# Optimization experiments

Hardware: AMD Instinct MI355X
Metric: run time of the kernel (lower is better)

Reference implementation:

```python
import jax, jax.numpy as jnp
import numpy as np

H = 256
W = 256
RADIUS = 1.5
TAU = 1.0
EPS = 1e-8


def _ndc_grid(h, w):
    ys, xs = jnp.meshgrid(jnp.arange(h, dtype=jnp.float32), jnp.arange(w, dtype=jnp.float32), indexing='ij')
    xs = xs / (w - 1) * 2.0 - 1.0
    ys = ys / (h - 1) * 2.0 - 1.0
    return jnp.stack([xs.ravel(), ys.ravel()], 0)  # [2, N]


def _make_rt(key, b, v):
    # near-identity extrinsics: identity rotation + small random translation
    t = jax.random.normal(key, (b, v, 3), dtype=jnp.float32) * 0.05
    rt = jnp.tile(jnp.eye(4, dtype=jnp.float32), (b, v, 1, 1))
    rt = rt.at[:, :, :3, 3].set(t)
    return rt


def setup_inputs() -> dict:
    key = jax.random.key(0)
    ks = jax.random.split(key, 4)
    B, V, C = 2, 3, 32
    depths = jax.random.uniform(ks[0], (B, V, 1, H, W), jnp.float32, 1.0, 3.0)
    feats = jax.random.normal(ks[1], (B, V, C, H, W), jnp.float32)
    K = jnp.tile(jnp.eye(4, dtype=jnp.float32), (B, 1, 1))
    K = K.at[:, 0, 0].set(1.2).at[:, 1, 1].set(1.2)  # NDC-space focal lengths
    src_RTs = _make_rt(ks[2], B, V)
    src_RTinvs = jnp.linalg.inv(src_RTs)
    dst_RTs = _make_rt(ks[3], B, 1)
    dst_RTinvs = jnp.linalg.inv(dst_RTs)
    return {"depths": depths, "feats": feats, "K": K, "src_RTs": src_RTs,
            "src_RTinvs": src_RTinvs, "dst_RTs": dst_RTs, "dst_RTinvs": dst_RTinvs}


def _view_to_world(depth, K_inv, RTinv):
    # depth: [BV, 1, N] -> world homogeneous coords [BV, 4, N]
    grid = _ndc_grid(H, W)                                      # [2, N]
    xy = grid[None] * depth                                     # [BV, 2, N]
    pc = jnp.concatenate([xy, depth, jnp.ones_like(depth)], 1)  # [BV, 4, N]
    cam = jnp.einsum('bij,bjn->bin', K_inv, pc)
    return jnp.einsum('bij,bjn->bin', RTinv, cam)


def _world_to_view(wrld, K, RT):
    cam = jnp.einsum('bij,bjn->bin', RT, wrld)
    proj = jnp.einsum('bij,bjn->bin', K, cam)
    z = proj[:, 2:3]
    xy = proj[:, 0:2] / (z + EPS)
    xy = jnp.where(z <= 0.0, -10.0, xy)       # invalid points pushed off-screen
    return jnp.concatenate([xy, z], 1)        # [BV, 3, N]


def _splatter(pc, feats, radius):
    # pc: [BV, N, 3] (x_ndc, y_ndc, depth); feats: [BV, C, N]
    BV, N, _ = pc.shape
    C = feats.shape[1]
    x, y, z = pc[..., 0], pc[..., 1], pc[..., 2]
    px = (x + 1.0) * 0.5 * (W - 1)
    py = (y + 1.0) * 0.5 * (H - 1)
    offs = jnp.array([[dy, dx] for dy in (-1, 0, 1) for dx in (-1, 0, 1)], dtype=jnp.float32)
    ix = jnp.round(px)[..., None] + offs[:, 1]     # [BV, N, 9]
    iy = jnp.round(py)[..., None] + offs[:, 0]
    dist = jnp.sqrt((ix - px[..., None]) ** 2 + (iy - py[..., None]) ** 2 + EPS)
    w_r = jnp.maximum(0.0, 1.0 - dist / radius)    # radius-based falloff
    valid = (ix >= 0) & (ix < W) & (iy >= 0) & (iy < H) & (z[..., None] > 0)
    w_d = jnp.exp(-TAU * z)[..., None]             # depth-aware (soft z-buffer) weight
    w = w_r * w_d * valid.astype(w_r.dtype)        # [BV, N, 9]
    idx = iy.astype(jnp.int32).clip(0, H - 1) * W + ix.astype(jnp.int32).clip(0, W - 1)
    flat = (jnp.arange(BV, dtype=jnp.int32)[:, None, None] * (H * W) + idx).reshape(-1)
    w_sum = jax.ops.segment_sum(w.reshape(-1), flat, num_segments=BV * H * W)
    fw = (feats[:, :, :, None] * w[:, None, :, :]).transpose(0, 2, 3, 1).reshape(-1, C)
    f_sum = jax.ops.segment_sum(fw, flat, num_segments=BV * H * W)
    z_sum = jax.ops.segment_sum((z[..., None] * w).reshape(-1), flat, num_segments=BV * H * W)
    out_f = (f_sum / (w_sum[:, None] + EPS)).reshape(BV, H, W, C).transpose(0, 3, 1, 2)
    out_d = (z_sum / (w_sum + EPS)).reshape(BV, 1, H, W)
    return out_f, out_d


def reference(depths, feats, K, src_RTs, src_RTinvs, dst_RTs, dst_RTinvs):
    B, V, C = feats.shape[0], feats.shape[1], feats.shape[2]
    N = H * W
    d = depths.reshape(B * V, 1, N)
    f = feats.reshape(B * V, C, N)
    K_bv = jnp.repeat(K, V, axis=0)
    K_inv_bv = jnp.repeat(jnp.linalg.inv(K), V, axis=0)
    src_rtinv = src_RTinvs.reshape(B * V, 4, 4)
    dst_rt = jnp.repeat(dst_RTs[:, 0], V, axis=0)
    wrld = _view_to_world(d, K_inv_bv, src_rtinv)      # view -> world per source view
    sampler = _world_to_view(wrld, K_bv, dst_rt)       # world -> target view [BV,3,N]
    pc = sampler.transpose(0, 2, 1)                    # [BV, N, 3]
    prj_f, prj_d = _splatter(pc, f, RADIUS)
    return prj_f.reshape(B, V, C, H, W), prj_d.reshape(B, V, 1, H, W)
```

## Files before the change

kernel.cpp:

```cpp
#include <hip/hip_runtime.h>
#include <hip/hip_fp16.h>
#include <math.h>

#define H 256
#define W 256
#define HW (H * W)
#define B 2
#define V 3
#define BV (B * V)
#define C 32
#define RADIUS 1.5f
#define TAU 1.0f
#define EPS 1e-8f

#define NPIX (BV * HW)
#define NBLK (NPIX / 256)

#define GW 258
#define GH 258
#define NCELL (BV * GH * GW)
#define NSUMS ((NCELL + 255) / 256)
#define ROWCAP 64

__device__ __forceinline__ int swizzle_block(int bid) {
    return (bid & 7) * (NBLK / 8) + (bid >> 3);
}

__global__ void setup_kernel(const float* __restrict__ Kmat,
                             const float* __restrict__ srcRTinv,
                             const float* __restrict__ dstRT,
                             float* __restrict__ Mbuf) {
    int bv = threadIdx.x;
    if (bv >= BV) return;
    int b = bv / V;

    float a[4][8];
    for (int i = 0; i < 4; i++)
        for (int j = 0; j < 4; j++) {
            a[i][j] = Kmat[b * 16 + i * 4 + j];
            a[i][4 + j] = (i == j) ? 1.0f : 0.0f;
        }
    for (int col = 0; col < 4; col++) {
        int piv = col;
        float best = fabsf(a[col][col]);
        for (int r = col + 1; r < 4; r++) {
            float v = fabsf(a[r][col]);
            if (v > best) { best = v; piv = r; }
        }
        if (piv != col) {
            for (int j = 0; j < 8; j++) {
                float t = a[col][j]; a[col][j] = a[piv][j]; a[piv][j] = t;
            }
        }
        float s = 1.0f / a[col][col];
        for (int j = 0; j < 8; j++) a[col][j] *= s;
        for (int r = 0; r < 4; r++) {
            if (r == col) continue;
            float m = a[r][col];
            for (int j = 0; j < 8; j++) a[r][j] -= m * a[col][j];
        }
    }
    float Kinv[16];
    for (int i = 0; i < 4; i++)
        for (int j = 0; j < 4; j++) Kinv[i * 4 + j] = a[i][4 + j];

    float T1[16];
    const float* S = srcRTinv + bv * 16;
    for (int i = 0; i < 4; i++)
        for (int j = 0; j < 4; j++) {
            float acc = 0.0f;
            for (int k = 0; k < 4; k++) acc += S[i * 4 + k] * Kinv[k * 4 + j];
            T1[i * 4 + j] = acc;
        }
    float T2[16];
    const float* D = dstRT + b * 16;
    for (int i = 0; i < 4; i++)
        for (int j = 0; j < 4; j++) {
            float acc = 0.0f;
            for (int k = 0; k < 4; k++) acc += D[i * 4 + k] * T1[k * 4 + j];
            T2[i * 4 + j] = acc;
        }
    const float* Kb = Kmat + b * 16;
    for (int i = 0; i < 4; i++)
        for (int j = 0; j < 4; j++) {
            float acc = 0.0f;
            for (int k = 0; k < 4; k++) acc += Kb[i * 4 + k] * T2[k * 4 + j];
            Mbuf[bv * 16 + i * 4 + j] = acc;
        }
}

__global__ __launch_bounds__(256) void project_count_kernel(
    const float* __restrict__ depths, const float* __restrict__ Mbuf,
    float4* __restrict__ staging, int2* __restrict__ meta) {
    int gid = swizzle_block(blockIdx.x) * 256 + threadIdx.x;
    int bv = gid >> 16;
    int n = gid & (HW - 1);

    float xn = (float)(n & (W - 1)) * (2.0f / (W - 1)) - 1.0f;
    float yn = (float)(n >> 8)      * (2.0f / (H - 1)) - 1.0f;
    float d = depths[gid];
    const float* M = Mbuf + bv * 16;
    float X = xn * d, Y = yn * d;
    float p0 = M[0] * X + M[1] * Y + M[2] * d + M[3];
    float p1 = M[4] * X + M[5] * Y + M[6] * d + M[7];
    float z  = M[8] * X + M[9] * Y + M[10] * d + M[11];

    int cell = -1;
    float px = 0.0f, py = 0.0f;
    if (z > 0.0f) {
        float inv = 1.0f / (z + EPS);
        px = (p0 * inv + 1.0f) * 0.5f * (float)(W - 1);
        py = (p1 * inv + 1.0f) * 0.5f * (float)(H - 1);
        float rx = rintf(px), ry = rintf(py);
        if (rx >= -1.0f && rx <= (float)W && ry >= -1.0f && ry <= (float)H) {
            cell = bv * (GH * GW) + ((int)ry + 1) * GW + ((int)rx + 1);
            atomicAdd(&meta[cell].y, 1);
        }
    }
    staging[gid] = make_float4(px, py, z, __int_as_float(cell));
}

__global__ __launch_bounds__(256) void alloc1_kernel(int2* __restrict__ meta,
                                                     int* __restrict__ bsum) {
    int i = blockIdx.x * 256 + threadIdx.x;
    int c = (i < NCELL) ? meta[i].y : 0;
    int lane = threadIdx.x & 63;
    int wid = threadIdx.x >> 6;
    int x = c;
#pragma unroll
    for (int dlt = 1; dlt < 64; dlt <<= 1) {
        int y = __shfl_up(x, dlt);
        if (lane >= dlt) x += y;
    }
    __shared__ int wsum[4];
    __shared__ int wbase[4];
    if (lane == 63) wsum[wid] = x;
    __syncthreads();
    if (threadIdx.x == 0) {
        int s0 = wsum[0], s1 = wsum[1], s2 = wsum[2], s3 = wsum[3];
        wbase[0] = 0; wbase[1] = s0; wbase[2] = s0 + s1; wbase[3] = s0 + s1 + s2;
        bsum[blockIdx.x] = s0 + s1 + s2 + s3;
    }
    __syncthreads();
    if (i <= NCELL) meta[i].x = wbase[wid] + (x - c);
}

__global__ __launch_bounds__(256) void alloc2_kernel(int* __restrict__ bsum) {
    __shared__ int wsum[4];
    __shared__ int wbase[4];
    __shared__ int carry_s;
    int tid = threadIdx.x;
    int lane = tid & 63;
    int wid = tid >> 6;
    if (tid == 0) carry_s = 0;
    __syncthreads();
    const int nchunk = (NSUMS + 255) / 256;
    for (int ch = 0; ch < nchunk; ch++) {
        int i = ch * 256 + tid;
        int c = (i < NSUMS) ? bsum[i] : 0;
        int x = c;
#pragma unroll
        for (int dlt = 1; dlt < 64; dlt <<= 1) {
            int y = __shfl_up(x, dlt);
            if (lane >= dlt) x += y;
        }
        if (lane == 63) wsum[wid] = x;
        __syncthreads();
        if (tid == 0) {
            int cr = carry_s;
            int s0 = wsum[0], s1 = wsum[1], s2 = wsum[2], s3 = wsum[3];
            wbase[0] = cr; wbase[1] = cr + s0; wbase[2] = cr + s0 + s1;
            wbase[3] = cr + s0 + s1 + s2;
            carry_s = cr + s0 + s1 + s2 + s3;
        }
        __syncthreads();
        if (i < NSUMS) bsum[i] = wbase[wid] + (x - c);
        __syncthreads();
    }
}

__global__ __launch_bounds__(256) void fill_kernel(
    const float* __restrict__ feats, const float4* __restrict__ staging,
    const int* __restrict__ bsum, int2* __restrict__ meta,
    float4* __restrict__ entries16, uint4* __restrict__ entriesF) {
    __shared__ float sm[C][257];
    int blk = blockIdx.x;
    int bv = blk >> 8;
    int n0 = (blk & 255) << 8;
    int tid = threadIdx.x;
    const float* src = feats + (size_t)bv * C * HW + n0;
#pragma unroll
    for (int c = 0; c < C; c++) sm[c][tid] = src[(size_t)c * HW + tid];
    __syncthreads();

    int gid = (bv << 16) | (n0 + tid);
    float4 s = staging[gid];
    int cell = __float_as_int(s.w);
    if (cell < 0) return;
    int pos = bsum[cell >> 8] + atomicAdd(&meta[cell].x, 1);

    float wd = expf(-TAU * s.z);
    entries16[pos] = make_float4(s.x, s.y, s.z, wd);

    uint4* dst = entriesF + (size_t)pos * 4;
#pragma unroll
    for (int g = 0; g < 4; g++) {
        __half2 h0 = __floats2half2_rn(sm[g * 8 + 0][tid], sm[g * 8 + 1][tid]);
        __half2 h1 = __floats2half2_rn(sm[g * 8 + 2][tid], sm[g * 8 + 3][tid]);
        __half2 h2 = __floats2half2_rn(sm[g * 8 + 4][tid], sm[g * 8 + 5][tid]);
        __half2 h3 = __floats2half2_rn(sm[g * 8 + 6][tid], sm[g * 8 + 7][tid]);
        uint4 pk;
        pk.x = *(unsigned int*)&h0;
        pk.y = *(unsigned int*)&h1;
        pk.z = *(unsigned int*)&h2;
        pk.w = *(unsigned int*)&h3;
        dst[g] = pk;
    }
}

__global__ __launch_bounds__(256) void gather_kernel(
    const float4* __restrict__ entries16, const uint4* __restrict__ entriesF,
    const int2* __restrict__ meta, const int* __restrict__ bsum,
    float* __restrict__ out) {
    __shared__ float4 lds_e[18][ROWCAP];
    __shared__ int cs_s[18][19];
    __shared__ int row_rs[18];
    __shared__ int row_stg[18];

    int sblk = swizzle_block(blockIdx.x);
    int bv = sblk >> 8;
    int t = sblk & 255;
    int ty0 = (t >> 4) << 4;
    int tx0 = (t & 15) << 4;
    int tid = threadIdx.x;
    int cellbase = bv * (GH * GW);

    for (int i = tid; i < 18 * 19; i += 256) {
        int hr = i / 19, lc = i - hr * 19;
        int cg = cellbase + (ty0 + hr) * GW + (tx0 + lc);
        int2 m = meta[cg];
        cs_s[hr][lc] = bsum[cg >> 8] + m.x - m.y;
    }
    __syncthreads();
    if (tid < 18) {
        int rs = cs_s[tid][0];
        row_rs[tid] = rs;
        row_stg[tid] = min(cs_s[tid][18] - rs, ROWCAP);
    }
    __syncthreads();
    {
        int wid = tid >> 6, lane = tid & 63;
        for (int hr = wid; hr < 18; hr += 4)
            if (lane < row_stg[hr])
                lds_e[hr][lane] = entries16[row_rs[hr] + lane];
    }
    __syncthreads();

    int lx = tid & 15, ly = tid >> 4;
    float qx = (float)(tx0 + lx);
    float qy = (float)(ty0 + ly);

    float wsum = 0.0f, zwsum = 0.0f;
    float facc[C];
#pragma unroll
    for (int c = 0; c < C; c++) facc[c] = 0.0f;

    auto accum = [&](float4 v, int pos) {
        float ddx = qx - v.x, ddy = qy - v.y;
        float d2 = ddx * ddx + ddy * ddy + EPS;
        if (d2 < RADIUS * RADIUS) {
            float dist = sqrtf(d2);
            float wr = 1.0f - dist * (1.0f / RADIUS);
            float w = wr * v.w;
            wsum += w;
            zwsum += v.z * w;
            const uint4* fp = entriesF + (size_t)pos * 4;
#pragma unroll
            for (int g = 0; g < 4; g++) {
                uint4 fv = fp[g];
                const __half2* h2 = (const __half2*)&fv;
#pragma unroll
                for (int k = 0; k < 4; k++) {
                    float2 f2 = __half22float2(h2[k]);
                    facc[g * 8 + 2 * k]     = fmaf(w, f2.x, facc[g * 8 + 2 * k]);
                    facc[g * 8 + 2 * k + 1] = fmaf(w, f2.y, facc[g * 8 + 2 * k + 1]);
                }
            }
        }
    };

#pragma unroll
    for (int dy = 0; dy < 3; dy++) {
        int hr = ly + dy;
        int s = cs_s[hr][lx];
        int e = cs_s[hr][lx + 3];
        int rs = row_rs[hr];
        int se = rs + row_stg[hr];
        int e1 = min(e, se);
        for (int pos = s; pos < e1; ++pos)
            accum(lds_e[hr][pos - rs], pos);
        for (int pos = max(s, se); pos < e; ++pos)
            accum(entries16[pos], pos);
    }

    int q = ((ty0 + ly) << 8) | (tx0 + lx);
    int gid = (bv << 16) | q;
    float invw = 1.0f / (wsum + EPS);
    float* ob = out + (size_t)bv * C * HW + q;
#pragma unroll
    for (int c = 0; c < C; c++) ob[(size_t)c * HW] = facc[c] * invw;
    out[(size_t)BV * C * HW + gid] = zwsum * invw;
}

extern "C" void kernel_launch(void* const* d_in, const int* in_sizes, int n_in,
                              void* d_out, int out_size, void* d_ws, size_t ws_size,
                              hipStream_t stream) {
    const float* depths   = (const float*)d_in[0];
    const float* feats    = (const float*)d_in[1];
    const float* Kmat     = (const float*)d_in[2];
    const float* srcRTinv = (const float*)d_in[4];
    const float* dstRT    = (const float*)d_in[5];
    float* out = (float*)d_out;

    char* ws = (char*)d_ws;
    size_t off_entriesF = 0;
    size_t off_entries16 = off_entriesF + (size_t)NPIX * 64;
    size_t off_staging = off_entries16 + (size_t)NPIX * 16;
    size_t off_meta = off_staging + (size_t)NPIX * 16;
    size_t off_bsum = off_meta + (size_t)(NCELL + 1) * 8;
    size_t off_M = off_bsum + (size_t)NSUMS * 4 + 16;
    size_t needed = off_M + (size_t)BV * 16 * 4;

    if (ws_size < needed) {
        hipMemsetAsync(d_out, 0, (size_t)out_size * 4, stream);
        return;
    }

    uint4* entriesF   = (uint4*)(ws + off_entriesF);
    float4* entries16 = (float4*)(ws + off_entries16);
    float4* staging   = (float4*)(ws + off_staging);
    int2* meta        = (int2*)(ws + off_meta);
    int* bsum         = (int*)(ws + off_bsum);
    float* Mbuf       = (float*)(ws + off_M);

    hipMemsetAsync(meta, 0, (size_t)(NCELL + 1) * 8, stream);
    setup_kernel<<<1, 64, 0, stream>>>(Kmat, srcRTinv, dstRT, Mbuf);
    project_count_kernel<<<NBLK, 256, 0, stream>>>(depths, Mbuf, staging, meta);
    alloc1_kernel<<<NSUMS, 256, 0, stream>>>(meta, bsum);
    alloc2_kernel<<<1, 256, 0, stream>>>(bsum);
    fill_kernel<<<NBLK, 256, 0, stream>>>(feats, staging, bsum, meta,
                                          entries16, entriesF);
    gather_kernel<<<NBLK, 256, 0, stream>>>(entries16, entriesF, meta, bsum,
                                            out);
}
```

Before: 183.9 us.

## Stage half-precision splat features into LDS alongside positions in gather kernel

The gather kernel now stages each tile's entry features (fp16, 64 bytes per entry, padded to a stride of 5 uint4) in shared memory next to the positions. Entries are packed into one flat buffer of up to 384 entries with per-row offsets, instead of a fixed 64 entries per row. This is meant to replace repeated scattered global feature reads by neighbouring threads with LDS reads. In exchange it uses about 36KB of LDS per block, which may lower occupancy, and it adds a serial prefix computation on one thread.

New measurement: 183.6 us. No clear change (-0.2%).

```diff
diff --git a/kernel.cpp b/kernel.cpp
--- a/kernel.cpp
+++ b/kernel.cpp
@@ -20,7 +20,7 @@
 #define GH 258
 #define NCELL (BV * GH * GW)
 #define NSUMS ((NCELL + 255) / 256)
-#define ROWCAP 64
+#define ECAP 384
 
 __device__ __forceinline__ int swizzle_block(int bid) {
     return (bid & 7) * (NBLK / 8) + (bid >> 3);
@@ -222,10 +222,12 @@
     const float4* __restrict__ entries16, const uint4* __restrict__ entriesF,
     const int2* __restrict__ meta, const int* __restrict__ bsum,
     float* __restrict__ out) {
-    __shared__ float4 lds_e[18][ROWCAP];
     __shared__ int cs_s[18][19];
     __shared__ int row_rs[18];
-    __shared__ int row_stg[18];
+    __shared__ int row_off[18];
+    __shared__ int row_sl[18];
+    __shared__ float4 lds_e[ECAP];
+    __shared__ uint4 lds_f[ECAP * 5];
 
     int sblk = swizzle_block(blockIdx.x);
     int bv = sblk >> 8;
@@ -242,17 +244,30 @@
         cs_s[hr][lc] = bsum[cg >> 8] + m.x - m.y;
     }
     __syncthreads();
-    if (tid < 18) {
-        int rs = cs_s[tid][0];
-        row_rs[tid] = rs;
-        row_stg[tid] = min(cs_s[tid][18] - rs, ROWCAP);
+    if (tid == 0) {
+        int off = 0;
+        for (int hr = 0; hr < 18; hr++) {
+            int rs = cs_s[hr][0];
+            int len = cs_s[hr][18] - rs;
+            int sl = min(len, ECAP - off);
+            if (sl < 0) sl = 0;
+            row_rs[hr] = rs;
+            row_off[hr] = off;
+            row_sl[hr] = sl;
+            off += sl;
+        }
     }
     __syncthreads();
     {
         int wid = tid >> 6, lane = tid & 63;
-        for (int hr = wid; hr < 18; hr += 4)
-            if (lane < row_stg[hr])
-                lds_e[hr][lane] = entries16[row_rs[hr] + lane];
+        for (int hr = wid; hr < 18; hr += 4) {
+            int rs = row_rs[hr], off = row_off[hr], sl = row_sl[hr];
+            for (int j = lane; j < sl; j += 64)
+                lds_e[off + j] = entries16[rs + j];
+            int j0 = lane >> 2, g = lane & 3;
+            for (int j = j0; j < sl; j += 16)
+                lds_f[(off + j) * 5 + g] = entriesF[(size_t)(rs + j) * 4 + g];
+        }
     }
     __syncthreads();
 
@@ -265,7 +280,29 @@
 #pragma unroll
     for (int c = 0; c < C; c++) facc[c] = 0.0f;
 
-    auto accum = [&](float4 v, int pos) {
+    auto accum_lds = [&](float4 v, int li) {
+        float ddx = qx - v.x, ddy = qy - v.y;
+        float d2 = ddx * ddx + ddy * ddy + EPS;
+        if (d2 < RADIUS * RADIUS) {
+            float dist = sqrtf(d2);
+            float wr = 1.0f - dist * (1.0f / RADIUS);
+            float w = wr * v.w;
+            wsum += w;
+            zwsum += v.z * w;
+#pragma unroll
+            for (int g = 0; g < 4; g++) {
+                uint4 fv = lds_f[li * 5 + g];
+                const __half2* h2 = (const __half2*)&fv;
+#pragma unroll
+                for (int k = 0; k < 4; k++) {
+                    float2 f2 = __half22float2(h2[k]);
+                    facc[g * 8 + 2 * k]     = fmaf(w, f2.x, facc[g * 8 + 2 * k]);
+                    facc[g * 8 + 2 * k + 1] = fmaf(w, f2.y, facc[g * 8 + 2 * k + 1]);
+                }
+            }
+        }
+    };
+    auto accum_glb = [&](float4 v, int pos) {
         float ddx = qx - v.x, ddy = qy - v.y;
         float d2 = ddx * ddx + ddy * ddy + EPS;
         if (d2 < RADIUS * RADIUS) {
@@ -295,12 +332,15 @@
         int s = cs_s[hr][lx];
         int e = cs_s[hr][lx + 3];
         int rs = row_rs[hr];
-        int se = rs + row_stg[hr];
-        int e1 = min(e, se);
-        for (int pos = s; pos < e1; ++pos)
-            accum(lds_e[hr][pos - rs], pos);
-        for (int pos = max(s, se); pos < e; ++pos)
-            accum(entries16[pos], pos);
+        int off = row_off[hr];
+        int sEnd = rs + row_sl[hr];
+        int e1 = min(e, sEnd);
+        for (int pos = s; pos < e1; ++pos) {
+            int li = off + (pos - rs);
+            accum_lds(lds_e[li], li);
+        }
+        for (int pos = max(s, sEnd); pos < e; ++pos)
+            accum_glb(entries16[pos], pos);
     }
 
     int q = ((ty0 + ly) << 8) | (tx0 + lx);
```
